# Optimization experiments

Measured on AMD Instinct MI355X. Metric: run time of the kernel, lower is better.

Reference implementation:

```python
import jax, jax.numpy as jnp
import numpy as np

B = 8192          # batch
DIM = 2048        # feature dim
FANOUT = 10       # balanced 10-ary tree, depth 3 -> 1000 leaves
N_NODES = 1 + 10 + 100  # inner nodes with classifiers = 111
NUM_CLASSES = 1000


def setup_inputs() -> dict:
    key = jax.random.key(0)
    k1, k2, k3, k4 = jax.random.split(key, 4)
    x = jax.random.normal(k1, (B, DIM), dtype=jnp.float32)
    labels = jax.random.randint(k2, (B,), 0, NUM_CLASSES, dtype=jnp.int64 if jax.config.jax_enable_x64 else jnp.int32)
    # Stacked per-node Linear(dim, num_child+1): column 0 is the extra slot
    # included in the softmax but never routed to (children use cols 1..FANOUT).
    W = jax.random.normal(k3, (N_NODES, DIM, FANOUT + 1), dtype=jnp.float32) * (1.0 / np.sqrt(DIM))
    b = jax.random.normal(k4, (N_NODES, FANOUT + 1), dtype=jnp.float32) * 0.01
    return {"x": x, "labels": labels, "W": W, "b": b}


def reference(x, labels, W, b):
    # All 111 tiny per-node Linear+softmax classifiers fused into one batched GEMM.
    logits = jnp.einsum('bd,ndk->bnk', x, W) + b          # [B, 111, 11]
    probs = jax.nn.softmax(logits, axis=-1)               # softmax over num_child+1 (incl. dummy col 0)
    # Hierarchical path probabilities (root.path_prob = 1.0):
    # level-1 nodes are children of root (node 0), via softmax columns 1..10.
    p1 = probs[:, 0, 1:]                                   # [B, 10]
    # level-2 nodes: children of nodes 1..10
    p2 = (p1[:, :, None] * probs[:, 1:11, 1:]).reshape(x.shape[0], 100)    # [B, 100]
    # leaves: children of nodes 11..110 -> 1000 classes (out[:, 1:] slice already applied)
    out = (p2[:, :, None] * probs[:, 11:111, 1:]).reshape(x.shape[0], NUM_CLASSES)  # [B, 1000]
    penalty = jnp.float32(0.0)
    return (out, penalty)
```

## Files before the change

kernel.cpp:

```cpp
#include <hip/hip_runtime.h>
#include <hip/hip_bf16.h>
#include <hip/hip_fp16.h>

typedef _Float16 f16;
typedef __attribute__((ext_vector_type(8))) _Float16 f16x8;
typedef __attribute__((ext_vector_type(4))) float f32x4;

#define DIM     2048
#define BROWS   8192
#define NCOLS   1221
#define NPAD    1280
#define NNODES  111
#define BM      128
#define BN      128
#define BK      64
#define NKT     (DIM / BK)
#define MT      (BROWS / BM)
#define NT      (NPAD / BN)

__global__ __launch_bounds__(256) void prep_x(const float* __restrict__ X,
                                              f16* __restrict__ Xf) {
    __shared__ float T[128 * 68];
    int blk = blockIdx.x;
    int mt = blk >> 5, kt = blk & 31;
    int t = threadIdx.x;
    int row = t >> 1, half = t & 1;
    const float* src = X + (size_t)(mt * 128 + row) * DIM + kt * 64 + half * 32;
    float* dst = T + row * 68 + half * 32;
    #pragma unroll
    for (int i = 0; i < 8; ++i) ((f32x4*)dst)[i] = ((const f32x4*)src)[i];
    __syncthreads();
    int w = t >> 6, l = t & 63, r = l & 15, q = l >> 4;
    f16* out = Xf + (size_t)blk * 8192;
    #pragma unroll
    for (int p = 0; p < 4; ++p) {
        int gk = p * 4 + w;
        int kk = gk >> 3, g = gk & 7;
        const float* s = T + (g * 16 + r) * 68 + kk * 32 + q * 8;
        f32x4 a = *(const f32x4*)s;
        f32x4 b = *(const f32x4*)(s + 4);
        f16x8 h;
        h[0] = (f16)a[0]; h[1] = (f16)a[1]; h[2] = (f16)a[2]; h[3] = (f16)a[3];
        h[4] = (f16)b[0]; h[5] = (f16)b[1]; h[6] = (f16)b[2]; h[7] = (f16)b[3];
        *(f16x8*)(out + (size_t)(p * 256 + t) * 8) = h;
    }
}

__global__ void prep_b(const float* __restrict__ W, f16* __restrict__ Bf) {
    int idx = blockIdx.x * 256 + threadIdx.x;
    int c = idx & 1023, img = idx >> 10;
    int nt = img >> 5, kt = img & 31;
    int kk = c >> 9, g = (c >> 6) & 7, l = c & 63, r = l & 15, q = l >> 4;
    int col = nt * 128 + g * 16 + r;
    int d0  = kt * 64 + kk * 32 + q * 8;
    f16x8 v;
    if (col < NCOLS) {
        int n = col / 11, k = col - n * 11;
        const float* src = W + ((size_t)n * DIM + d0) * 11 + k;
        #pragma unroll
        for (int e = 0; e < 8; ++e) v[e] = (f16)src[(size_t)e * 11];
    } else {
        #pragma unroll
        for (int e = 0; e < 8; ++e) v[e] = (f16)0.f;
    }
    *(f16x8*)(Bf + (size_t)idx * 8) = v;
}

__global__ __launch_bounds__(512, 4) void gemm_f16(const f16* __restrict__ Xf,
                                                   const f16* __restrict__ Bf,
                                                   f16* __restrict__ Lh) {
    __shared__ __align__(16) f16 As[8192];
    __shared__ __align__(16) f16 Bs[8192];

    int bid = blockIdx.x;
    int swz = (bid & 7) * 80 + (bid >> 3);
    int mt = swz / 10, nt = swz - mt * 10;

    int t = threadIdx.x, w = t >> 6, l = t & 63, r = l & 15, q = l >> 4;
    int wm = w >> 2, wn = w & 3;

    const f16* abase = Xf + (size_t)(mt * 32) * 8192 + (size_t)t * 8;
    const f16* bbase = Bf + (size_t)(nt * 32) * 8192 + (size_t)t * 8;

    f32x4 acc[4][2];
    #pragma unroll
    for (int i = 0; i < 4; ++i)
        #pragma unroll
        for (int j = 0; j < 2; ++j) acc[i][j] = (f32x4)0.f;

    for (int kt = 0; kt < NKT; ++kt) {
        __syncthreads();
        const f16* asrc = abase + (size_t)kt * 8192;
        const f16* bsrc = bbase + (size_t)kt * 8192;
        #pragma unroll
        for (int p = 0; p < 2; ++p) {
            __builtin_amdgcn_global_load_lds(
                (const __attribute__((address_space(1))) void*)(asrc + p * 4096),
                (__attribute__((address_space(3))) void*)(As + p * 4096 + w * 512),
                16, 0, 0);
            __builtin_amdgcn_global_load_lds(
                (const __attribute__((address_space(1))) void*)(bsrc + p * 4096),
                (__attribute__((address_space(3))) void*)(Bs + p * 4096 + w * 512),
                16, 0, 0);
        }
        __syncthreads();
        #pragma unroll
        for (int kk = 0; kk < 2; ++kk) {
            f16x8 af[4], bf[2];
            #pragma unroll
            for (int m = 0; m < 4; ++m)
                af[m] = *(const f16x8*)(As + ((size_t)((kk * 8 + wm * 4 + m) * 64 + l)) * 8);
            #pragma unroll
            for (int n = 0; n < 2; ++n)
                bf[n] = *(const f16x8*)(Bs + ((size_t)((kk * 8 + wn * 2 + n) * 64 + l)) * 8);
            #pragma unroll
            for (int m = 0; m < 4; ++m)
                #pragma unroll
                for (int n = 0; n < 2; ++n)
                    acc[m][n] = __builtin_amdgcn_mfma_f32_16x16x32_f16(af[m], bf[n], acc[m][n], 0, 0, 0);
        }
    }

    #pragma unroll
    for (int m = 0; m < 4; ++m) {
        int row = mt * 128 + wm * 64 + m * 16 + q * 4;
        #pragma unroll
        for (int n = 0; n < 2; ++n) {
            int col = nt * 128 + wn * 32 + n * 16 + r;
            #pragma unroll
            for (int j = 0; j < 4; ++j)
                Lh[(size_t)(row + j) * NPAD + col] = (f16)acc[m][n][j];
        }
    }
}

__global__ void tree_epi(const f16* __restrict__ L, const float* __restrict__ bias,
                         float* __restrict__ out) {
    __shared__ float P[4][NNODES * 11];
    int w = threadIdx.x >> 6, l = threadIdx.x & 63;
    int row = blockIdx.x * 4 + w;
    const f16* Lr = L + (size_t)row * NPAD;

    for (int n = l; n < NNODES; n += 64) {
        float v[11], mx = -1e30f;
        #pragma unroll
        for (int k = 0; k < 11; ++k) { v[k] = (float)Lr[n * 11 + k] + bias[n * 11 + k]; mx = fmaxf(mx, v[k]); }
        float s = 0.f;
        #pragma unroll
        for (int k = 0; k < 11; ++k) { v[k] = __expf(v[k] - mx); s += v[k]; }
        float inv = 1.f / s;
        #pragma unroll
        for (int k = 0; k < 11; ++k) P[w][n * 11 + k] = v[k] * inv;
    }
    __syncthreads();
    const float* Pw = P[w];
    for (int c = l; c < 1000; c += 64) {
        int i  = c / 100;
        int j  = (c % 100) / 10;
        int mm = c % 10;
        float p = Pw[1 + i] * Pw[(1 + i) * 11 + 1 + j] * Pw[(11 + 10 * i + j) * 11 + 1 + mm];
        out[(size_t)row * 1000 + c] = p;
    }
    if (row == 0 && threadIdx.x == 0) out[(size_t)BROWS * 1000] = 0.f;
}

extern "C" void kernel_launch(void* const* d_in, const int* in_sizes, int n_in,
                              void* d_out, int out_size, void* d_ws, size_t ws_size,
                              hipStream_t stream) {
    const float* x    = (const float*)d_in[0];
    const float* W    = (const float*)d_in[2];
    const float* bias = (const float*)d_in[3];
    float* out = (float*)d_out;

    f16* Xf = (f16*)d_ws;
    f16* Bf = (f16*)((char*)d_ws + 33554432);
    f16* Lh = (f16*)((char*)d_ws + 38797312);

    prep_x <<<MT * NKT, 256, 0, stream>>>(x, Xf);
    prep_b <<<1280, 256, 0, stream>>>(W, Bf);
    gemm_f16<<<MT * NT, 512, 0, stream>>>(Xf, Bf, Lh);
    tree_epi<<<BROWS / 4, 256, 0, stream>>>(Lh, bias, out);
}
```

Measured before the change: 87.62 us.

## Double-buffer GEMM LDS tiles with BK=32 and stage epilogue logits rows in LDS

The GEMM main loop becomes a two-stage software pipeline. It uses ping-pong LDS buffers with a K step of 32, so the global-to-LDS load of the next tile overlaps the MFMA work on the current one, with explicit waitcnt and barrier placement. The launch-bounds occupancy hint is dropped. Separately, the tree epilogue copies each row's f16 logits into shared memory with vectorized 16-byte loads before the softmax, replacing strided scalar global reads. The prepacked layout still matches, since each 64-wide packed tile splits into two 32-wide halves. Halving BK doubles the number of barriers per tile.

```diff
diff --git a/kernel.cpp b/kernel.cpp
--- a/kernel.cpp
+++ b/kernel.cpp
@@ -13,7 +13,7 @@
 #define NNODES  111
 #define BM      128
 #define BN      128
-#define BK      64
+#define BK      32
 #define NKT     (DIM / BK)
 #define MT      (BROWS / BM)
 #define NT      (NPAD / BN)
@@ -66,11 +66,11 @@
     *(f16x8*)(Bf + (size_t)idx * 8) = v;
 }
 
-__global__ __launch_bounds__(512, 4) void gemm_f16(const f16* __restrict__ Xf,
-                                                   const f16* __restrict__ Bf,
-                                                   f16* __restrict__ Lh) {
-    __shared__ __align__(16) f16 As[8192];
-    __shared__ __align__(16) f16 Bs[8192];
+__global__ __launch_bounds__(512) void gemm_f16(const f16* __restrict__ Xf,
+                                                const f16* __restrict__ Bf,
+                                                f16* __restrict__ Lh) {
+    __shared__ __align__(16) f16 As[2][4096];
+    __shared__ __align__(16) f16 Bs[2][4096];
 
     int bid = blockIdx.x;
     int swz = (bid & 7) * 80 + (bid >> 3);
@@ -79,8 +79,8 @@
     int t = threadIdx.x, w = t >> 6, l = t & 63, r = l & 15, q = l >> 4;
     int wm = w >> 2, wn = w & 3;
 
-    const f16* abase = Xf + (size_t)(mt * 32) * 8192 + (size_t)t * 8;
-    const f16* bbase = Bf + (size_t)(nt * 32) * 8192 + (size_t)t * 8;
+    const f16* abase = Xf + (size_t)mt * 262144 + (size_t)t * 8;
+    const f16* bbase = Bf + (size_t)nt * 262144 + (size_t)t * 8;
 
     f32x4 acc[4][2];
     #pragma unroll
@@ -88,38 +88,53 @@
         #pragma unroll
         for (int j = 0; j < 2; ++j) acc[i][j] = (f32x4)0.f;
 
-    for (int kt = 0; kt < NKT; ++kt) {
-        __syncthreads();
-        const f16* asrc = abase + (size_t)kt * 8192;
-        const f16* bsrc = bbase + (size_t)kt * 8192;
-        #pragma unroll
-        for (int p = 0; p < 2; ++p) {
-            __builtin_amdgcn_global_load_lds(
-                (const __attribute__((address_space(1))) void*)(asrc + p * 4096),
-                (__attribute__((address_space(3))) void*)(As + p * 4096 + w * 512),
-                16, 0, 0);
-            __builtin_amdgcn_global_load_lds(
-                (const __attribute__((address_space(1))) void*)(bsrc + p * 4096),
-                (__attribute__((address_space(3))) void*)(Bs + p * 4096 + w * 512),
-                16, 0, 0);
-        }
-        __syncthreads();
-        #pragma unroll
-        for (int kk = 0; kk < 2; ++kk) {
-            f16x8 af[4], bf[2];
-            #pragma unroll
-            for (int m = 0; m < 4; ++m)
-                af[m] = *(const f16x8*)(As + ((size_t)((kk * 8 + wm * 4 + m) * 64 + l)) * 8);
-            #pragma unroll
-            for (int n = 0; n < 2; ++n)
-                bf[n] = *(const f16x8*)(Bs + ((size_t)((kk * 8 + wn * 2 + n) * 64 + l)) * 8);
-            #pragma unroll
-            for (int m = 0; m < 4; ++m)
-                #pragma unroll
-                for (int n = 0; n < 2; ++n)
-                    acc[m][n] = __builtin_amdgcn_mfma_f32_16x16x32_f16(af[m], bf[n], acc[m][n], 0, 0, 0);
-        }
-    }
+#define STAGE(KT, C)                                                             \
+    {                                                                            \
+        __builtin_amdgcn_global_load_lds(                                        \
+            (const __attribute__((address_space(1))) void*)(abase + (size_t)(KT) * 4096), \
+            (__attribute__((address_space(3))) void*)(&As[C][w * 512]), 16, 0, 0);        \
+        __builtin_amdgcn_global_load_lds(                                        \
+            (const __attribute__((address_space(1))) void*)(bbase + (size_t)(KT) * 4096), \
+            (__attribute__((address_space(3))) void*)(&Bs[C][w * 512]), 16, 0, 0);        \
+    }
+
+#define COMPUTE(C)                                                               \
+    {                                                                            \
+        f16x8 af[4], bfr[2];                                                     \
+        _Pragma("unroll")                                                        \
+        for (int m = 0; m < 4; ++m)                                              \
+            af[m] = *(const f16x8*)(&As[C][((wm * 4 + m) * 64 + l) * 8]);        \
+        _Pragma("unroll")                                                        \
+        for (int n = 0; n < 2; ++n)                                              \
+            bfr[n] = *(const f16x8*)(&Bs[C][((wn * 2 + n) * 64 + l) * 8]);       \
+        _Pragma("unroll")                                                        \
+        for (int m = 0; m < 4; ++m)                                              \
+            _Pragma("unroll")                                                    \
+            for (int n = 0; n < 2; ++n)                                          \
+                acc[m][n] = __builtin_amdgcn_mfma_f32_16x16x32_f16(af[m], bfr[n], acc[m][n], 0, 0, 0); \
+    }
+
+    STAGE(0, 0)
+
+    #pragma unroll 2
+    for (int kt = 0; kt < NKT - 1; ++kt) {
+        int cc = kt & 1, cn = cc ^ 1;
+        STAGE(kt + 1, cn)
+        asm volatile("s_waitcnt vmcnt(2)" ::: "memory");
+        __builtin_amdgcn_s_barrier();
+        asm volatile("" ::: "memory");
+        COMPUTE(cc)
+        asm volatile("s_waitcnt lgkmcnt(0)" ::: "memory");
+        __builtin_amdgcn_s_barrier();
+        asm volatile("" ::: "memory");
+    }
+    asm volatile("s_waitcnt vmcnt(0)" ::: "memory");
+    __builtin_amdgcn_s_barrier();
+    asm volatile("" ::: "memory");
+    COMPUTE(1)
+
+#undef STAGE
+#undef COMPUTE
 
     #pragma unroll
     for (int m = 0; m < 4; ++m) {
@@ -137,14 +152,20 @@
 __global__ void tree_epi(const f16* __restrict__ L, const float* __restrict__ bias,
                          float* __restrict__ out) {
     __shared__ float P[4][NNODES * 11];
+    __shared__ f16 R[4][NPAD];
     int w = threadIdx.x >> 6, l = threadIdx.x & 63;
     int row = blockIdx.x * 4 + w;
-    const f16* Lr = L + (size_t)row * NPAD;
+
+    const f16x8* src = (const f16x8*)(L + (size_t)row * NPAD);
+    f16x8* dst = (f16x8*)R[w];
+    dst[l]      = src[l];
+    dst[l + 64] = src[l + 64];
+    if (l < 32) dst[l + 128] = src[l + 128];
 
     for (int n = l; n < NNODES; n += 64) {
         float v[11], mx = -1e30f;
         #pragma unroll
-        for (int k = 0; k < 11; ++k) { v[k] = (float)Lr[n * 11 + k] + bias[n * 11 + k]; mx = fmaxf(mx, v[k]); }
+        for (int k = 0; k < 11; ++k) { v[k] = (float)R[w][n * 11 + k] + bias[n * 11 + k]; mx = fmaxf(mx, v[k]); }
         float s = 0.f;
         #pragma unroll
         for (int k = 0; k < 11; ++k) { v[k] = __expf(v[k] - mx); s += v[k]; }
@@ -176,7 +197,7 @@
     f16* Bf = (f16*)((char*)d_ws + 33554432);
     f16* Lh = (f16*)((char*)d_ws + 38797312);
 
-    prep_x <<<MT * NKT, 256, 0, stream>>>(x, Xf);
+    prep_x <<<MT * 32, 256, 0, stream>>>(x, Xf);
     prep_b <<<1280, 256, 0, stream>>>(W, Bf);
     gemm_f16<<<MT * NT, 512, 0, stream>>>(Xf, Bf, Lh);
     tree_epi<<<BROWS / 4, 256, 0, stream>>>(Lh, bias, out);
```

Measured after the change: 106.9 us. +22.0%, slower.
